# Kernel optimization log

Measured on AMD Instinct MI355X. Metric: run time of the kernel, lower is better.

Reference implementation:

```python
import jax, jax.numpy as jnp
import numpy as np

DIM = 384
HEADS = 12
WH, WW = 8, 10
N = WH * WW  # tokens per window


def _rel_tables():
    # continuous relative coords table, log-spaced (Swin-v2 style, as in source)
    ch = np.arange(-(WH - 1), WH, dtype=np.float32)
    cw = np.arange(-(WW - 1), WW, dtype=np.float32)
    t = np.stack(np.meshgrid(ch, cw, indexing='ij'), axis=-1)  # (2WH-1, 2WW-1, 2)
    t[..., 0] /= (WH - 1)
    t[..., 1] /= (WW - 1)
    t *= 8.0
    t = np.sign(t) * np.log2(np.abs(t) + 1.0) / np.log2(8.0)
    # relative position index (N, N)
    coords = np.stack(np.meshgrid(np.arange(WH), np.arange(WW), indexing='ij'))
    flat = coords.reshape(2, -1)
    rel = (flat[:, :, None] - flat[:, None, :]).transpose(1, 2, 0)
    rel[..., 0] += WH - 1
    rel[..., 1] += WW - 1
    rel[..., 0] *= 2 * WW - 1
    idx = rel.sum(-1)
    return jnp.asarray(t.reshape(-1, 2)), jnp.asarray(idx.reshape(-1))


def _layernorm(x, g, b):
    m = x.mean(-1, keepdims=True)
    v = ((x - m) ** 2).mean(-1, keepdims=True)
    return (x - m) * jax.lax.rsqrt(v + 1e-5) * g + b


def setup_inputs() -> dict:
    key = jax.random.key(0)
    ks = jax.random.split(key, 8)
    s = 0.02
    return {
        'x': jax.random.normal(ks[0], (16, 96, 120, DIM), jnp.float32),
        'norm1_g': jnp.ones((DIM,), jnp.float32),
        'norm1_b': jnp.zeros((DIM,), jnp.float32),
        'qkv_w': jax.random.normal(ks[1], (3 * DIM, DIM), jnp.float32) * s,
        'q_bias': jnp.zeros((DIM,), jnp.float32),
        'v_bias': jnp.zeros((DIM,), jnp.float32),
        'cpb_w1': jax.random.normal(ks[2], (512, 2), jnp.float32) * s,
        'cpb_b1': jnp.zeros((512,), jnp.float32),
        'cpb_w2': jax.random.normal(ks[3], (HEADS, 512), jnp.float32) * s,
        'proj_w': jax.random.normal(ks[4], (DIM, DIM), jnp.float32) * s,
        'proj_b': jnp.zeros((DIM,), jnp.float32),
        'ls1_g': jnp.full((DIM,), 1e-5, jnp.float32),
        'norm2_g': jnp.ones((DIM,), jnp.float32),
        'norm2_b': jnp.zeros((DIM,), jnp.float32),
        'glu_w': jax.random.normal(ks[5], (2048, DIM), jnp.float32) * s,
        'glu_b': jnp.zeros((2048,), jnp.float32),
        'out_w': jax.random.normal(ks[6], (DIM, 1024), jnp.float32) * s,
        'out_b': jnp.zeros((DIM,), jnp.float32),
        'ls2_g': jnp.full((DIM,), 1e-5, jnp.float32),
    }


def reference(x, norm1_g, norm1_b, qkv_w, q_bias, v_bias, cpb_w1, cpb_b1, cpb_w2,
              proj_w, proj_b, ls1_g, norm2_g, norm2_b, glu_w, glu_b, out_w, out_b, ls2_g):
    B, H, W, C = x.shape
    table, idx = _rel_tables()
    # ---- attention branch: norm -> window partition -> MHSA w/ cpb -> reverse ----
    y = _layernorm(x, norm1_g, norm1_b)
    win = y.reshape(B, H // WH, WH, W // WW, WW, C).transpose(0, 1, 3, 2, 4, 5).reshape(-1, N, C)
    qkv_b = jnp.concatenate([q_bias, jnp.zeros_like(v_bias), v_bias])
    qkv = win @ qkv_w.T + qkv_b                                  # (B_, N, 3C)
    qkv = qkv.reshape(-1, N, 3, HEADS, C // HEADS).transpose(2, 0, 3, 1, 4)
    q, k, v = qkv[0], qkv[1], qkv[2]                             # (B_, h, N, d)
    q = q.astype(jnp.float32)
    k = k.astype(jnp.float32)
    q = q / (jnp.linalg.norm(q, axis=-1, keepdims=True) + 5e-5)  # custom_normalize eps
    k = k / (jnp.linalg.norm(k, axis=-1, keepdims=True) + 5e-5)
    attn = jnp.einsum('bhnd,bhmd->bhnm', q, k)
    # continuous relative-position bias: 2-layer MLP over coords table, then gather
    bias_tab = jax.nn.relu(table @ cpb_w1.T + cpb_b1) @ cpb_w2.T     # (T, heads)
    bias = bias_tab[idx].reshape(N, N, HEADS).transpose(2, 0, 1)     # (heads, N, N)
    attn = jax.nn.softmax(attn + 16.0 * jax.nn.sigmoid(bias)[None], axis=-1).astype(x.dtype)
    o = jnp.einsum('bhnm,bhmd->bhnd', attn, v).transpose(0, 2, 1, 3).reshape(-1, N, C)
    o = o @ proj_w.T + proj_b
    o = o.reshape(B, H // WH, W // WW, WH, WW, C).transpose(0, 1, 3, 2, 4, 5).reshape(B, H, W, C)
    x = x + ls1_g * o
    # ---- gated MLP branch ----
    y = _layernorm(x, norm2_g, norm2_b)
    p = y @ glu_w.T + glu_b
    a, gate = jnp.split(p, 2, axis=-1)
    h = a * jax.nn.gelu(gate, approximate=False)
    x = x + ls2_g * (h @ out_w.T + out_b)
    return x
```

## Files before the change

kernel.cpp:

```cpp
#include <hip/hip_runtime.h>
#include <hip/hip_bf16.h>
#include <stdint.h>
#include <math.h>

using bf16 = __hip_bfloat16;
typedef __attribute__((ext_vector_type(8))) short short8;
typedef __attribute__((ext_vector_type(4))) short short4b;
typedef __attribute__((ext_vector_type(4))) float f32x4;

#define TOK    184320
#define CDIM   384
#define NWIN   2304
#define NTOK   80
#define HEADS  12
#define BK     64

constexpr size_t R0_SZ    = (size_t)TOK * CDIM * 2;
constexpr size_t R0_OFF   = 0;
constexpr size_t Q_OFF    = R0_SZ;
constexpr size_t K_OFF    = Q_OFF + R0_SZ;
constexpr size_t V_OFF    = K_OFF + R0_SZ;
constexpr size_t BIAS_OFF = V_OFF + R0_SZ;
constexpr size_t WQKV_OFF = BIAS_OFF + (size_t)HEADS * 6400 * 4;
constexpr size_t WPROJ_OFF= WQKV_OFF + (size_t)1152 * 384 * 2;
constexpr size_t WGLU_OFF = WPROJ_OFF + (size_t)384 * 384 * 2;
constexpr size_t WOUT_OFF = WGLU_OFF + (size_t)2048 * 384 * 2;

__device__ __forceinline__ float b2f(unsigned short u) {
  return __uint_as_float(((unsigned)u) << 16);
}
__device__ __forceinline__ short f2bs(float x) {
  return (short)__bfloat16_as_ushort(__float2bfloat16(x));
}

__device__ __forceinline__ void gload_lds16(const void* g, void* l) {
  typedef __attribute__((address_space(1))) char gchar;
  typedef __attribute__((address_space(3))) char lchar;
  __builtin_amdgcn_global_load_lds((gchar*)(uintptr_t)g, (lchar*)(uintptr_t)l, 16, 0, 0);
}

__device__ __forceinline__ int xcd_swz(int orig, int nwg) {
  int q = nwg >> 3, r = nwg & 7;
  int xcd = orig & 7, loc = orig >> 3;
  return (xcd < r ? xcd * (q + 1) : r * (q + 1) + (xcd - r) * q) + loc;
}

__device__ __forceinline__ int token_to_winrow(int t) {
  int b  = t / (96 * 120);
  int r  = t - b * (96 * 120);
  int hh = r / 120, ww = r - (r / 120) * 120;
  int win = b * 144 + (hh >> 3) * 12 + (ww / 10);
  int n   = (hh & 7) * 10 + (ww % 10);
  return win * NTOK + n;
}

__device__ __forceinline__ int winrow_to_token(int row) {
  int win = row / NTOK, n = row - win * NTOK;
  int b = win / 144, rem = win - b * 144;
  int hh = (rem / 12) * 8 + n / 10;
  int ww = (rem % 12) * 10 + n % 10;
  return (b * 96 + hh) * 120 + ww;
}

__global__ void cvt_f32_bf16(const float* __restrict__ in, bf16* __restrict__ out, int n) {
  int i = blockIdx.x * 256 + threadIdx.x;
  if (i < n) out[i] = __float2bfloat16(in[i]);
}

__global__ void cpb_bias_kernel(const float* __restrict__ w1, const float* __restrict__ b1,
                                const float* __restrict__ w2, float* __restrict__ biasT) {
  __shared__ float tab[285][12];
  for (int r = threadIdx.x; r < 285; r += blockDim.x) {
    int i = r / 19, j = r - (r / 19) * 19;
    float c0 = 8.0f * (float)(i - 7) / 7.0f;
    float c1 = 8.0f * (float)(j - 9) / 9.0f;
    const float inv3 = 1.0f / 3.0f;
    float t0 = (c0 >= 0.f ? 1.f : -1.f) * log2f(fabsf(c0) + 1.f) * inv3;
    float t1 = (c1 >= 0.f ? 1.f : -1.f) * log2f(fabsf(c1) + 1.f) * inv3;
    float acc[12];
    #pragma unroll
    for (int h = 0; h < 12; h++) acc[h] = 0.f;
    for (int k = 0; k < 512; k++) {
      float hk = fmaxf(w1[2 * k] * t0 + w1[2 * k + 1] * t1 + b1[k], 0.f);
      #pragma unroll
      for (int h = 0; h < 12; h++) acc[h] += hk * w2[h * 512 + k];
    }
    #pragma unroll
    for (int h = 0; h < 12; h++) tab[r][h] = acc[h];
  }
  __syncthreads();
  for (int e = threadIdx.x; e < 6400; e += blockDim.x) {
    int n = e / 80, m = e - (e / 80) * 80;
    int id = (n / 10 - m / 10 + 7) * 19 + (n % 10 - m % 10 + 9);
    #pragma unroll
    for (int h = 0; h < 12; h++) {
      float t = tab[id][h];
      biasT[h * 6400 + m * 80 + n] = 16.0f / (1.0f + __expf(-t));
    }
  }
}

__global__ __launch_bounds__(256)
void ln_kernel(const float* __restrict__ x, const float* __restrict__ g,
               const float* __restrict__ b, bf16* __restrict__ out, int windowed) {
  const int wv = threadIdx.x >> 6, lane = threadIdx.x & 63;
  const int token = blockIdx.x * 4 + wv;
  const float* px = x + (size_t)token * CDIM;
  float v[6];
  float s = 0.f;
  #pragma unroll
  for (int j = 0; j < 6; j++) { v[j] = px[lane + 64 * j]; s += v[j]; }
  #pragma unroll
  for (int off = 32; off; off >>= 1) s += __shfl_xor(s, off);
  const float mean = s * (1.0f / 384.0f);
  float sq = 0.f;
  #pragma unroll
  for (int j = 0; j < 6; j++) { float d = v[j] - mean; sq += d * d; }
  #pragma unroll
  for (int off = 32; off; off >>= 1) sq += __shfl_xor(sq, off);
  const float rs = rsqrtf(sq * (1.0f / 384.0f) + 1e-5f);
  const int rowb = windowed ? token_to_winrow(token) : token;
  bf16* po = out + (size_t)rowb * CDIM;
  #pragma unroll
  for (int j = 0; j < 6; j++) {
    int c = lane + 64 * j;
    po[c] = __float2bfloat16((v[j] - mean) * rs * g[c] + b[c]);
  }
}

__global__ __launch_bounds__(64)
void vtrans_kernel(const bf16* __restrict__ v, bf16* __restrict__ vT) {
  __shared__ unsigned short vt[32][82];
  const int wh = blockIdx.x, t = threadIdx.x;
  const unsigned short* vg = (const unsigned short*)v + (size_t)wh * 2560;
  #pragma unroll
  for (int j = 0; j < 5; j++) {
    int c = (t + 64 * j) * 8;
    short8 u = *(const short8*)(vg + c);
    int n = c >> 5, d = c & 31;
    #pragma unroll
    for (int e = 0; e < 8; e++) vt[d + e][n] = (unsigned short)u[e];
  }
  __syncthreads();
  unsigned int* og = (unsigned int*)((unsigned short*)vT + (size_t)wh * 2560);
  #pragma unroll
  for (int j = 0; j < 20; j++) {
    int p = t + 64 * j;
    int e = p * 2;
    int d = e / 80, kcol = e - (e / 80) * 80;
    og[p] = (unsigned int)vt[d][kcol] | ((unsigned int)vt[d][kcol + 1] << 16);
  }
}

#define STAGE_A(buf, kt)                                                          \
  _Pragma("unroll")                                                               \
  for (int j_ = 0; j_ < 4; j_++) {                                                \
    const int ch_ = j_ * 8 + w;                                                   \
    const int el_ = ch_ * 512 + lane * 8;                                         \
    gload_lds16(Ab + (size_t)(el_ >> 6) * LDA + (kt) + (el_ & 63),                \
                As[buf] + ch_ * 512);                                             \
  }
#define STAGE_B(Bp, Bls, buf, kt)                                                 \
  _Pragma("unroll")                                                               \
  for (int j_ = 0; j_ < 2; j_++) {                                                \
    const int ch_ = j_ * 8 + w;                                                   \
    const int el_ = ch_ * 512 + lane * 8;                                         \
    gload_lds16(Bp + (size_t)(el_ >> 6) * LDA + (kt) + (el_ & 63),                \
                Bls[buf] + ch_ * 512);                                            \
  }

#define FRAG_IDX(base, m16, kk) ((base) + ((m16) + lr) * 64 + (kk) + kg * 8)

#define GEMM2_BODY(K_, NT_)                                                       \
  const int LDA = K_;                                                             \
  const int w = threadIdx.x >> 6, lane = threadIdx.x & 63;                        \
  const int wr = w >> 1, wc = w & 1, lr = lane & 15, kg = lane >> 4;              \
  f32x4 acc[4][4];                                                                \
  _Pragma("unroll")                                                               \
  for (int m = 0; m < 4; m++)                                                     \
    _Pragma("unroll")                                                             \
    for (int n = 0; n < 4; n++) acc[m][n] = (f32x4){0.f, 0.f, 0.f, 0.f};          \
  STAGE_A(0, 0) STAGE_B(Bb, Bs, 0, 0)                                             \
  __syncthreads();                                                                \
  for (int t = 0; t < NT_; t++) {                                                 \
    const int cur = t & 1;                                                        \
    if (t + 1 < NT_) { STAGE_A(cur ^ 1, (t + 1) * BK) STAGE_B(Bb, Bs, cur ^ 1, (t + 1) * BK) } \
    _Pragma("unroll")                                                             \
    for (int kk = 0; kk < BK; kk += 32) {                                         \
      short8 af[4], bfr[4];                                                       \
      _Pragma("unroll")                                                           \
      for (int m = 0; m < 4; m++)                                                 \
        af[m] = *(const short8*)FRAG_IDX(As[cur], wr * 64 + m * 16, kk);          \
      _Pragma("unroll")                                                           \
      for (int n = 0; n < 4; n++)                                                 \
        bfr[n] = *(const short8*)FRAG_IDX(Bs[cur], wc * 64 + n * 16, kk);         \
      _Pragma("unroll")                                                           \
      for (int m = 0; m < 4; m++)                                                 \
        _Pragma("unroll")                                                         \
        for (int n = 0; n < 4; n++)                                               \
          acc[m][n] = __builtin_amdgcn_mfma_f32_16x16x32_bf16(af[m], bfr[n], acc[m][n], 0, 0, 0); \
    }                                                                             \
    if (t + 1 < NT_) __syncthreads();                                             \
  }

__global__ __launch_bounds__(512, 2)
void gemm_qkv_kernel(const bf16* __restrict__ A, const bf16* __restrict__ W,
                     const float* __restrict__ qb, const float* __restrict__ vb,
                     bf16* __restrict__ qo, bf16* __restrict__ ko, bf16* __restrict__ vo) {
  __shared__ bf16 As[2][256 * 64], Bs[2][128 * 64];
  const int nbx = 9;
  const int swz = xcd_swz(blockIdx.x, gridDim.x);
  const int by = swz / nbx, bx = swz - (swz / nbx) * nbx;
  const bf16* Ab = A + (size_t)by * 256 * 384;
  const bf16* Bb = W + (size_t)bx * 128 * 384;
  GEMM2_BODY(384, 6)
  #pragma unroll
  for (int m = 0; m < 4; m++)
    #pragma unroll
    for (int i = 0; i < 4; i++) {
      const int row = by * 256 + wr * 64 + m * 16 + kg * 4 + i;
      const int win = row / NTOK, n = row - win * NTOK;
      #pragma unroll
      for (int nn = 0; nn < 4; nn++) {
        const int col = bx * 128 + wc * 64 + nn * 16 + lr;
        const int which = col / 384;
        const int c = col - which * 384;
        const int head = c >> 5, d = c & 31;
        const size_t idx = (((size_t)win * HEADS + head) * NTOK + n) * 32 + d;
        float val = acc[m][nn][i];
        if (which == 0)      qo[idx] = __float2bfloat16(val + qb[c]);
        else if (which == 2) vo[idx] = __float2bfloat16(val + vb[c]);
        else                 ko[idx] = __float2bfloat16(val);
      }
    }
}

__global__ __launch_bounds__(512, 2)
void gemm_proj_kernel(const bf16* __restrict__ A, const bf16* __restrict__ W,
                      const float* __restrict__ pb, const float* __restrict__ x,
                      const float* __restrict__ ls1, float* __restrict__ out) {
  __shared__ bf16 As[2][256 * 64], Bs[2][128 * 64];
  const int nbx = 3;
  const int swz = xcd_swz(blockIdx.x, gridDim.x);
  const int by = swz / nbx, bx = swz - (swz / nbx) * nbx;
  const bf16* Ab = A + (size_t)by * 256 * 384;
  const bf16* Bb = W + (size_t)bx * 128 * 384;
  GEMM2_BODY(384, 6)
  #pragma unroll
  for (int m = 0; m < 4; m++)
    #pragma unroll
    for (int i = 0; i < 4; i++) {
      const int row = by * 256 + wr * 64 + m * 16 + kg * 4 + i;
      const int t = winrow_to_token(row);
      #pragma unroll
      for (int nn = 0; nn < 4; nn++) {
        const int col = bx * 128 + wc * 64 + nn * 16 + lr;
        const size_t gi = (size_t)t * CDIM + col;
        out[gi] = x[gi] + ls1[col] * (acc[m][nn][i] + pb[col]);
      }
    }
}

__global__ __launch_bounds__(512, 2)
void gemm_out_kernel(const bf16* __restrict__ A, const bf16* __restrict__ W,
                     const float* __restrict__ ob, const float* __restrict__ ls2,
                     float* __restrict__ out) {
  __shared__ bf16 As[2][256 * 64], Bs[2][128 * 64];
  const int nbx = 3;
  const int swz = xcd_swz(blockIdx.x, gridDim.x);
  const int by = swz / nbx, bx = swz - (swz / nbx) * nbx;
  const bf16* Ab = A + (size_t)by * 256 * 1024;
  const bf16* Bb = W + (size_t)bx * 128 * 1024;
  GEMM2_BODY(1024, 16)
  #pragma unroll
  for (int m = 0; m < 4; m++)
    #pragma unroll
    for (int i = 0; i < 4; i++) {
      const int row = by * 256 + wr * 64 + m * 16 + kg * 4 + i;
      #pragma unroll
      for (int nn = 0; nn < 4; nn++) {
        const int col = bx * 128 + wc * 64 + nn * 16 + lr;
        const size_t gi = (size_t)row * CDIM + col;
        out[gi] += ls2[col] * (acc[m][nn][i] + ob[col]);
      }
    }
}

__global__ __launch_bounds__(512, 2)
void gemm_glu_kernel(const bf16* __restrict__ A, const bf16* __restrict__ W,
                     const float* __restrict__ gb, bf16* __restrict__ h) {
  __shared__ bf16 As[2][256 * 64], Ba[2][128 * 64], Bg[2][128 * 64];
  const int nbx = 8;
  const int swz = xcd_swz(blockIdx.x, gridDim.x);
  const int by = swz / nbx, bx = swz - (swz / nbx) * nbx;
  const bf16* Ab = A + (size_t)by * 256 * 384;
  const bf16* Wa = W + (size_t)(bx * 128) * 384;
  const bf16* Wg = W + (size_t)(1024 + bx * 128) * 384;
  const int LDA = 384;
  const int w = threadIdx.x >> 6, lane = threadIdx.x & 63;
  const int wr = w >> 1, wc = w & 1, lr = lane & 15, kg = lane >> 4;
  f32x4 aA[4][4], aG[4][4];
  #pragma unroll
  for (int m = 0; m < 4; m++)
    #pragma unroll
    for (int n = 0; n < 4; n++) {
      aA[m][n] = (f32x4){0.f, 0.f, 0.f, 0.f};
      aG[m][n] = (f32x4){0.f, 0.f, 0.f, 0.f};
    }
  STAGE_A(0, 0) STAGE_B(Wa, Ba, 0, 0) STAGE_B(Wg, Bg, 0, 0)
  __syncthreads();
  for (int t = 0; t < 6; t++) {
    const int cur = t & 1;
    if (t + 1 < 6) {
      STAGE_A(cur ^ 1, (t + 1) * BK)
      STAGE_B(Wa, Ba, cur ^ 1, (t + 1) * BK)
      STAGE_B(Wg, Bg, cur ^ 1, (t + 1) * BK)
    }
    #pragma unroll
    for (int kk = 0; kk < BK; kk += 32) {
      short8 af[4], ba[4], bg2[4];
      #pragma unroll
      for (int m = 0; m < 4; m++)
        af[m] = *(const short8*)FRAG_IDX(As[cur], wr * 64 + m * 16, kk);
      #pragma unroll
      for (int n = 0; n < 4; n++) {
        ba[n]  = *(const short8*)FRAG_IDX(Ba[cur], wc * 64 + n * 16, kk);
        bg2[n] = *(const short8*)FRAG_IDX(Bg[cur], wc * 64 + n * 16, kk);
      }
      #pragma unroll
      for (int m = 0; m < 4; m++)
        #pragma unroll
        for (int n = 0; n < 4; n++) {
          aA[m][n] = __builtin_amdgcn_mfma_f32_16x16x32_bf16(af[m], ba[n],  aA[m][n], 0, 0, 0);
          aG[m][n] = __builtin_amdgcn_mfma_f32_16x16x32_bf16(af[m], bg2[n], aG[m][n], 0, 0, 0);
        }
    }
    if (t + 1 < 6) __syncthreads();
  }
  #pragma unroll
  for (int m = 0; m < 4; m++)
    #pragma unroll
    for (int i = 0; i < 4; i++) {
      const int row = by * 256 + wr * 64 + m * 16 + kg * 4 + i;
      #pragma unroll
      for (int nn = 0; nn < 4; nn++) {
        const int col = bx * 128 + wc * 64 + nn * 16 + lr;
        float a = aA[m][nn][i] + gb[col];
        float g = aG[m][nn][i] + gb[1024 + col];
        float gelu = 0.5f * g * (1.0f + erff(g * 0.70710678118654752f));
        h[(size_t)row * 1024 + col] = __float2bfloat16(a * gelu);
      }
    }
}

__global__ __launch_bounds__(256, 2)
void attn_kernel(const bf16* __restrict__ q, const bf16* __restrict__ k,
                 const bf16* __restrict__ vT, const float* __restrict__ biasT,
                 bf16* __restrict__ o) {
  __shared__ short P_all[4][80 * 104];
  const int wv = threadIdx.x >> 6, lane = threadIdx.x & 63;
  const int lr = lane & 15, kg = lane >> 4;
  const int win = blockIdx.x;
  short* P = &P_all[wv][0];
  #pragma unroll
  for (int j = 0; j < 10; j++) {
    int idx = lane + 64 * j;
    int r = idx >> 3, c = idx & 7;
    *(int*)(P + r * 104 + 80 + c * 2) = 0;
  }
  for (int hh = 0; hh < 3; hh++) {
    const int head = wv * 3 + hh;
    const size_t hb = ((size_t)win * HEADS + head) * 2560;
    short8 qf[5], kf[5];
    #pragma unroll
    for (int t5 = 0; t5 < 5; t5++) {
      const int roff = (t5 * 16 + lr) * 32 + kg * 8;
      {
        short8 u = *(const short8*)((const unsigned short*)q + hb + roff);
        float f[8]; float s = 0.f;
        #pragma unroll
        for (int j2 = 0; j2 < 8; j2++) { float x = b2f((unsigned short)u[j2]); f[j2] = x; s += x * x; }
        s += __shfl_xor(s, 16); s += __shfl_xor(s, 32);
        float sc = 1.0f / (sqrtf(s) + 5e-5f);
        short8 r8;
        #pragma unroll
        for (int j2 = 0; j2 < 8; j2++) r8[j2] = f2bs(f[j2] * sc);
        qf[t5] = r8;
      }
      {
        short8 u = *(const short8*)((const unsigned short*)k + hb + roff);
        float f[8]; float s = 0.f;
        #pragma unroll
        for (int j2 = 0; j2 < 8; j2++) { float x = b2f((unsigned short)u[j2]); f[j2] = x; s += x * x; }
        s += __shfl_xor(s, 16); s += __shfl_xor(s, 32);
        float sc = 1.0f / (sqrtf(s) + 5e-5f);
        short8 r8;
        #pragma unroll
        for (int j2 = 0; j2 < 8; j2++) r8[j2] = f2bs(f[j2] * sc);
        kf[t5] = r8;
      }
    }
    f32x4 st[5][5];
    #pragma unroll
    for (int a = 0; a < 5; a++)
      #pragma unroll
      for (int b = 0; b < 5; b++) st[a][b] = (f32x4){0.f, 0.f, 0.f, 0.f};
    #pragma unroll
    for (int a = 0; a < 5; a++)
      #pragma unroll
      for (int b = 0; b < 5; b++)
        st[a][b] = __builtin_amdgcn_mfma_f32_16x16x32_bf16(kf[a], qf[b], st[a][b], 0, 0, 0);
    const float* bh = biasT + head * 6400;
    #pragma unroll
    for (int a = 0; a < 5; a++)
      #pragma unroll
      for (int b = 0; b < 5; b++)
        #pragma unroll
        for (int i = 0; i < 4; i++)
          st[a][b][i] += bh[(a * 16 + kg * 4 + i) * 80 + b * 16 + lr];
    float inv[5];
    #pragma unroll
    for (int b = 0; b < 5; b++) {
      float mx = -1e30f;
      #pragma unroll
      for (int a = 0; a < 5; a++)
        #pragma unroll
        for (int i = 0; i < 4; i++) mx = fmaxf(mx, st[a][b][i]);
      mx = fmaxf(mx, __shfl_xor(mx, 16));
      mx = fmaxf(mx, __shfl_xor(mx, 32));
      float sm = 0.f;
      #pragma unroll
      for (int a = 0; a < 5; a++)
        #pragma unroll
        for (int i = 0; i < 4; i++) { float e = __expf(st[a][b][i] - mx); st[a][b][i] = e; sm += e; }
      sm += __shfl_xor(sm, 16); sm += __shfl_xor(sm, 32);
      inv[b] = 1.0f / sm;
    }
    #pragma unroll
    for (int a = 0; a < 5; a++)
      #pragma unroll
      for (int b = 0; b < 5; b++) {
        short4b pk;
        #pragma unroll
        for (int i = 0; i < 4; i++) pk[i] = f2bs(st[a][b][i] * inv[b]);
        *(short4b*)(P + (b * 16 + lr) * 104 + a * 16 + kg * 4) = pk;
      }
    const unsigned short* vh = (const unsigned short*)vT + hb;
    short8 vf[2][3];
    #pragma unroll
    for (int dt = 0; dt < 2; dt++)
      #pragma unroll
      for (int ks = 0; ks < 3; ks++) {
        const int kb = ks * 32 + ((ks == 2 && kg >= 2) ? 0 : kg * 8);
        vf[dt][ks] = *(const short8*)(vh + (dt * 16 + lr) * 80 + kb);
      }
    f32x4 oc[5][2];
    #pragma unroll
    for (int b = 0; b < 5; b++)
      #pragma unroll
      for (int dt = 0; dt < 2; dt++) oc[b][dt] = (f32x4){0.f, 0.f, 0.f, 0.f};
    #pragma unroll
    for (int b = 0; b < 5; b++) {
      short8 pa[3];
      #pragma unroll
      for (int ks = 0; ks < 3; ks++)
        pa[ks] = *(const short8*)(P + (b * 16 + lr) * 104 + ks * 32 + kg * 8);
      #pragma unroll
      for (int dt = 0; dt < 2; dt++)
        #pragma unroll
        for (int ks = 0; ks < 3; ks++)
          oc[b][dt] = __builtin_amdgcn_mfma_f32_16x16x32_bf16(pa[ks], vf[dt][ks], oc[b][dt], 0, 0, 0);
    }
    unsigned short* ob = (unsigned short*)o + (size_t)win * NTOK * CDIM + head * 32;
    #pragma unroll
    for (int b = 0; b < 5; b++)
      #pragma unroll
      for (int i = 0; i < 4; i++) {
        const int row = b * 16 + kg * 4 + i;
        #pragma unroll
        for (int dt = 0; dt < 2; dt++)
          ob[(size_t)row * CDIM + dt * 16 + lr] = (unsigned short)f2bs(oc[b][dt][i]);
      }
  }
}

extern "C" void kernel_launch(void* const* d_in, const int* in_sizes, int n_in,
                              void* d_out, int out_size, void* d_ws, size_t ws_size,
                              hipStream_t stream) {
  const float* x       = (const float*)d_in[0];
  const float* n1g     = (const float*)d_in[1];
  const float* n1b     = (const float*)d_in[2];
  const float* qkv_w   = (const float*)d_in[3];
  const float* q_bias  = (const float*)d_in[4];
  const float* v_bias  = (const float*)d_in[5];
  const float* cpb_w1  = (const float*)d_in[6];
  const float* cpb_b1  = (const float*)d_in[7];
  const float* cpb_w2  = (const float*)d_in[8];
  const float* proj_w  = (const float*)d_in[9];
  const float* proj_b  = (const float*)d_in[10];
  const float* ls1     = (const float*)d_in[11];
  const float* n2g     = (const float*)d_in[12];
  const float* n2b     = (const float*)d_in[13];
  const float* glu_w   = (const float*)d_in[14];
  const float* glu_b   = (const float*)d_in[15];
  const float* out_w   = (const float*)d_in[16];
  const float* out_b   = (const float*)d_in[17];
  const float* ls2     = (const float*)d_in[18];
  float* out = (float*)d_out;

  char* ws = (char*)d_ws;
  bf16* r0     = (bf16*)(ws + R0_OFF);
  bf16* q_buf  = (bf16*)(ws + Q_OFF);
  bf16* k_buf  = (bf16*)(ws + K_OFF);
  bf16* v_buf  = (bf16*)(ws + V_OFF);
  bf16* h_buf  = (bf16*)(ws + Q_OFF);
  float* biasT = (float*)(ws + BIAS_OFF);
  bf16* wqkv   = (bf16*)(ws + WQKV_OFF);
  bf16* wproj  = (bf16*)(ws + WPROJ_OFF);
  bf16* wglu   = (bf16*)(ws + WGLU_OFF);
  bf16* wout   = (bf16*)(ws + WOUT_OFF);

  cvt_f32_bf16<<<dim3((1152 * 384 + 255) / 256), 256, 0, stream>>>(qkv_w, wqkv, 1152 * 384);
  cvt_f32_bf16<<<dim3((384 * 384 + 255) / 256), 256, 0, stream>>>(proj_w, wproj, 384 * 384);
  cvt_f32_bf16<<<dim3((2048 * 384 + 255) / 256), 256, 0, stream>>>(glu_w, wglu, 2048 * 384);
  cvt_f32_bf16<<<dim3((384 * 1024 + 255) / 256), 256, 0, stream>>>(out_w, wout, 384 * 1024);

  cpb_bias_kernel<<<1, 256, 0, stream>>>(cpb_w1, cpb_b1, cpb_w2, biasT);

  ln_kernel<<<TOK / 4, 256, 0, stream>>>(x, n1g, n1b, r0, 1);

  gemm_qkv_kernel<<<720 * 9, 512, 0, stream>>>(r0, wqkv, q_bias, v_bias, q_buf, k_buf, v_buf);

  vtrans_kernel<<<NWIN * HEADS, 64, 0, stream>>>(v_buf, r0);

  attn_kernel<<<NWIN, 256, 0, stream>>>(q_buf, k_buf, r0, biasT, v_buf);

  gemm_proj_kernel<<<720 * 3, 512, 0, stream>>>(v_buf, wproj, proj_b, x, ls1, out);

  ln_kernel<<<TOK / 4, 256, 0, stream>>>(out, n2g, n2b, r0, 0);

  gemm_glu_kernel<<<720 * 8, 512, 0, stream>>>(r0, wglu, glu_b, h_buf);

  gemm_out_kernel<<<720 * 3, 512, 0, stream>>>(h_buf, wout, out_b, ls2, out);

  (void)in_sizes; (void)n_in; (void)out_size; (void)ws_size;
}
```

Before: 2.620 ms.

## Triple-buffer GEMM LDS pipeline with XOR swizzle and halve GLU row tile

Replaces double-buffered LDS staging in the four GEMM kernels with a three-stage ring. It waits with explicit vmcnt waits and s_barrier instead of __syncthreads each step, so global loads for tile t+2 overlap compute on tile t. Source columns are XOR-swizzled by row, which is meant to cut LDS bank conflicts on fragment reads. MFMA blocks are wrapped in s_setprio to favour the math waves. The GLU kernel moves to 128-row tiles and a doubled grid to keep triple-buffer LDS usage at two blocks per CU, which costs more reloads of the weight tiles.

```diff
diff --git a/kernel.cpp b/kernel.cpp
--- a/kernel.cpp
+++ b/kernel.cpp
@@ -61,6 +61,8 @@
   int ww = (rem % 12) * 10 + n % 10;
   return (b * 96 + hh) * 120 + ww;
 }
+
+#define SWZ_COL(c_, r_) ((c_) ^ (((r_) & 7) << 3))
 
 __global__ void cvt_f32_bf16(const float* __restrict__ in, bf16* __restrict__ out, int n) {
   int i = blockIdx.x * 256 + threadIdx.x;
@@ -152,26 +154,50 @@
   }
 }
 
-#define STAGE_A(buf, kt)                                                          \
+#define STAGE3_A(buf, kt)                                                         \
   _Pragma("unroll")                                                               \
   for (int j_ = 0; j_ < 4; j_++) {                                                \
     const int ch_ = j_ * 8 + w;                                                   \
     const int el_ = ch_ * 512 + lane * 8;                                         \
-    gload_lds16(Ab + (size_t)(el_ >> 6) * LDA + (kt) + (el_ & 63),                \
-                As[buf] + ch_ * 512);                                             \
-  }
-#define STAGE_B(Bp, Bls, buf, kt)                                                 \
+    const int r_ = el_ >> 6, c_ = el_ & 63;                                       \
+    gload_lds16(Ab + (size_t)r_ * LDA + (kt) + SWZ_COL(c_, r_),                   \
+                As3 + (buf) * (256 * 64) + ch_ * 512);                            \
+  }
+#define STAGE3_B(Bp, Bls, nb_, buf, kt)                                           \
   _Pragma("unroll")                                                               \
-  for (int j_ = 0; j_ < 2; j_++) {                                                \
+  for (int j_ = 0; j_ < (nb_); j_++) {                                            \
     const int ch_ = j_ * 8 + w;                                                   \
     const int el_ = ch_ * 512 + lane * 8;                                         \
-    gload_lds16(Bp + (size_t)(el_ >> 6) * LDA + (kt) + (el_ & 63),                \
-                Bls[buf] + ch_ * 512);                                            \
-  }
-
-#define FRAG_IDX(base, m16, kk) ((base) + ((m16) + lr) * 64 + (kk) + kg * 8)
-
-#define GEMM2_BODY(K_, NT_)                                                       \
+    const int r_ = el_ >> 6, c_ = el_ & 63;                                       \
+    gload_lds16(Bp + (size_t)r_ * LDA + (kt) + SWZ_COL(c_, r_),                   \
+                Bls + (buf) * (128 * 64) + ch_ * 512);                            \
+  }
+
+#define COMPUTE3(buf)                                                             \
+  {                                                                               \
+    const bf16* A_ = As3 + (buf) * (256 * 64);                                    \
+    const bf16* B_ = Bs3 + (buf) * (128 * 64);                                    \
+    _Pragma("unroll")                                                             \
+    for (int kk = 0; kk < BK; kk += 32) {                                         \
+      const int cs_ = SWZ_COL(kk + kg * 8, lr);                                   \
+      short8 af[4], bfr[4];                                                       \
+      _Pragma("unroll")                                                           \
+      for (int m = 0; m < 4; m++)                                                 \
+        af[m] = *(const short8*)(A_ + (wr * 64 + m * 16 + lr) * 64 + cs_);        \
+      _Pragma("unroll")                                                           \
+      for (int n = 0; n < 4; n++)                                                 \
+        bfr[n] = *(const short8*)(B_ + (wc * 64 + n * 16 + lr) * 64 + cs_);       \
+      __builtin_amdgcn_s_setprio(1);                                              \
+      _Pragma("unroll")                                                           \
+      for (int m = 0; m < 4; m++)                                                 \
+        _Pragma("unroll")                                                         \
+        for (int n = 0; n < 4; n++)                                               \
+          acc[m][n] = __builtin_amdgcn_mfma_f32_16x16x32_bf16(af[m], bfr[n], acc[m][n], 0, 0, 0); \
+      __builtin_amdgcn_s_setprio(0);                                              \
+    }                                                                             \
+  }
+
+#define GEMM3_BODY(K_, NT_)                                                       \
   const int LDA = K_;                                                             \
   const int w = threadIdx.x >> 6, lane = threadIdx.x & 63;                        \
   const int wr = w >> 1, wc = w & 1, lr = lane & 15, kg = lane >> 4;              \
@@ -180,40 +206,34 @@
   for (int m = 0; m < 4; m++)                                                     \
     _Pragma("unroll")                                                             \
     for (int n = 0; n < 4; n++) acc[m][n] = (f32x4){0.f, 0.f, 0.f, 0.f};          \
-  STAGE_A(0, 0) STAGE_B(Bb, Bs, 0, 0)                                             \
-  __syncthreads();                                                                \
-  for (int t = 0; t < NT_; t++) {                                                 \
-    const int cur = t & 1;                                                        \
-    if (t + 1 < NT_) { STAGE_A(cur ^ 1, (t + 1) * BK) STAGE_B(Bb, Bs, cur ^ 1, (t + 1) * BK) } \
-    _Pragma("unroll")                                                             \
-    for (int kk = 0; kk < BK; kk += 32) {                                         \
-      short8 af[4], bfr[4];                                                       \
-      _Pragma("unroll")                                                           \
-      for (int m = 0; m < 4; m++)                                                 \
-        af[m] = *(const short8*)FRAG_IDX(As[cur], wr * 64 + m * 16, kk);          \
-      _Pragma("unroll")                                                           \
-      for (int n = 0; n < 4; n++)                                                 \
-        bfr[n] = *(const short8*)FRAG_IDX(Bs[cur], wc * 64 + n * 16, kk);         \
-      _Pragma("unroll")                                                           \
-      for (int m = 0; m < 4; m++)                                                 \
-        _Pragma("unroll")                                                         \
-        for (int n = 0; n < 4; n++)                                               \
-          acc[m][n] = __builtin_amdgcn_mfma_f32_16x16x32_bf16(af[m], bfr[n], acc[m][n], 0, 0, 0); \
+  STAGE3_A(0, 0) STAGE3_B(Bb, Bs3, 2, 0, 0)                                       \
+  STAGE3_A(1, BK) STAGE3_B(Bb, Bs3, 2, 1, BK)                                     \
+  _Pragma("unroll")                                                               \
+  for (int t = 0; t < NT_ - 1; t++) {                                             \
+    asm volatile("s_waitcnt vmcnt(6)" ::: "memory");                              \
+    __builtin_amdgcn_s_barrier();                                                 \
+    if (t + 2 < NT_) {                                                            \
+      STAGE3_A((t + 2) % 3, (t + 2) * BK)                                         \
+      STAGE3_B(Bb, Bs3, 2, (t + 2) % 3, (t + 2) * BK)                             \
     }                                                                             \
-    if (t + 1 < NT_) __syncthreads();                                             \
-  }
+    COMPUTE3(t % 3)                                                               \
+  }                                                                               \
+  asm volatile("s_waitcnt vmcnt(0)" ::: "memory");                                \
+  __builtin_amdgcn_s_barrier();                                                   \
+  COMPUTE3((NT_ - 1) % 3)
 
 __global__ __launch_bounds__(512, 2)
 void gemm_qkv_kernel(const bf16* __restrict__ A, const bf16* __restrict__ W,
                      const float* __restrict__ qb, const float* __restrict__ vb,
                      bf16* __restrict__ qo, bf16* __restrict__ ko, bf16* __restrict__ vo) {
-  __shared__ bf16 As[2][256 * 64], Bs[2][128 * 64];
+  __shared__ __align__(16) bf16 As3[3 * 256 * 64];
+  __shared__ __align__(16) bf16 Bs3[3 * 128 * 64];
   const int nbx = 9;
   const int swz = xcd_swz(blockIdx.x, gridDim.x);
   const int by = swz / nbx, bx = swz - (swz / nbx) * nbx;
   const bf16* Ab = A + (size_t)by * 256 * 384;
   const bf16* Bb = W + (size_t)bx * 128 * 384;
-  GEMM2_BODY(384, 6)
+  GEMM3_BODY(384, 6)
   #pragma unroll
   for (int m = 0; m < 4; m++)
     #pragma unroll
@@ -239,13 +259,14 @@
 void gemm_proj_kernel(const bf16* __restrict__ A, const bf16* __restrict__ W,
                       const float* __restrict__ pb, const float* __restrict__ x,
                       const float* __restrict__ ls1, float* __restrict__ out) {
-  __shared__ bf16 As[2][256 * 64], Bs[2][128 * 64];
+  __shared__ __align__(16) bf16 As3[3 * 256 * 64];
+  __shared__ __align__(16) bf16 Bs3[3 * 128 * 64];
   const int nbx = 3;
   const int swz = xcd_swz(blockIdx.x, gridDim.x);
   const int by = swz / nbx, bx = swz - (swz / nbx) * nbx;
   const bf16* Ab = A + (size_t)by * 256 * 384;
   const bf16* Bb = W + (size_t)bx * 128 * 384;
-  GEMM2_BODY(384, 6)
+  GEMM3_BODY(384, 6)
   #pragma unroll
   for (int m = 0; m < 4; m++)
     #pragma unroll
@@ -265,13 +286,14 @@
 void gemm_out_kernel(const bf16* __restrict__ A, const bf16* __restrict__ W,
                      const float* __restrict__ ob, const float* __restrict__ ls2,
                      float* __restrict__ out) {
-  __shared__ bf16 As[2][256 * 64], Bs[2][128 * 64];
+  __shared__ __align__(16) bf16 As3[3 * 256 * 64];
+  __shared__ __align__(16) bf16 Bs3[3 * 128 * 64];
   const int nbx = 3;
   const int swz = xcd_swz(blockIdx.x, gridDim.x);
   const int by = swz / nbx, bx = swz - (swz / nbx) * nbx;
   const bf16* Ab = A + (size_t)by * 256 * 1024;
   const bf16* Bb = W + (size_t)bx * 128 * 1024;
-  GEMM2_BODY(1024, 16)
+  GEMM3_BODY(1024, 16)
   #pragma unroll
   for (int m = 0; m < 4; m++)
     #pragma unroll
@@ -289,59 +311,99 @@
 __global__ __launch_bounds__(512, 2)
 void gemm_glu_kernel(const bf16* __restrict__ A, const bf16* __restrict__ W,
                      const float* __restrict__ gb, bf16* __restrict__ h) {
-  __shared__ bf16 As[2][256 * 64], Ba[2][128 * 64], Bg[2][128 * 64];
+  __shared__ __align__(16) bf16 Asl[3 * 128 * 64];
+  __shared__ __align__(16) bf16 Bal[3 * 128 * 64];
+  __shared__ __align__(16) bf16 Bgl[3 * 128 * 64];
   const int nbx = 8;
   const int swz = xcd_swz(blockIdx.x, gridDim.x);
   const int by = swz / nbx, bx = swz - (swz / nbx) * nbx;
-  const bf16* Ab = A + (size_t)by * 256 * 384;
+  const bf16* Ab = A + (size_t)by * 128 * 384;
   const bf16* Wa = W + (size_t)(bx * 128) * 384;
   const bf16* Wg = W + (size_t)(1024 + bx * 128) * 384;
   const int LDA = 384;
   const int w = threadIdx.x >> 6, lane = threadIdx.x & 63;
   const int wr = w >> 1, wc = w & 1, lr = lane & 15, kg = lane >> 4;
-  f32x4 aA[4][4], aG[4][4];
-  #pragma unroll
-  for (int m = 0; m < 4; m++)
+  f32x4 aA[2][4], aG[2][4];
+  #pragma unroll
+  for (int m = 0; m < 2; m++)
     #pragma unroll
     for (int n = 0; n < 4; n++) {
       aA[m][n] = (f32x4){0.f, 0.f, 0.f, 0.f};
       aG[m][n] = (f32x4){0.f, 0.f, 0.f, 0.f};
     }
-  STAGE_A(0, 0) STAGE_B(Wa, Ba, 0, 0) STAGE_B(Wg, Bg, 0, 0)
-  __syncthreads();
-  for (int t = 0; t < 6; t++) {
-    const int cur = t & 1;
-    if (t + 1 < 6) {
-      STAGE_A(cur ^ 1, (t + 1) * BK)
-      STAGE_B(Wa, Ba, cur ^ 1, (t + 1) * BK)
-      STAGE_B(Wg, Bg, cur ^ 1, (t + 1) * BK)
-    }
+  STAGE3_B(Ab, Asl, 2, 0, 0) STAGE3_B(Wa, Bal, 2, 0, 0) STAGE3_B(Wg, Bgl, 2, 0, 0)
+  STAGE3_B(Ab, Asl, 2, 1, BK) STAGE3_B(Wa, Bal, 2, 1, BK) STAGE3_B(Wg, Bgl, 2, 1, BK)
+  #pragma unroll
+  for (int t = 0; t < 5; t++) {
+    asm volatile("s_waitcnt vmcnt(6)" ::: "memory");
+    __builtin_amdgcn_s_barrier();
+    if (t + 2 < 6) {
+      STAGE3_B(Ab, Asl, 2, (t + 2) % 3, (t + 2) * BK)
+      STAGE3_B(Wa, Bal, 2, (t + 2) % 3, (t + 2) * BK)
+      STAGE3_B(Wg, Bgl, 2, (t + 2) % 3, (t + 2) * BK)
+    }
+    {
+      const bf16* A_ = Asl + (t % 3) * (128 * 64);
+      const bf16* Ba_ = Bal + (t % 3) * (128 * 64);
+      const bf16* Bg_ = Bgl + (t % 3) * (128 * 64);
+      #pragma unroll
+      for (int kk = 0; kk < BK; kk += 32) {
+        const int cs_ = SWZ_COL(kk + kg * 8, lr);
+        short8 af[2], ba[4], bg2[4];
+        #pragma unroll
+        for (int m = 0; m < 2; m++)
+          af[m] = *(const short8*)(A_ + (wr * 32 + m * 16 + lr) * 64 + cs_);
+        #pragma unroll
+        for (int n = 0; n < 4; n++) {
+          ba[n]  = *(const short8*)(Ba_ + (wc * 64 + n * 16 + lr) * 64 + cs_);
+          bg2[n] = *(const short8*)(Bg_ + (wc * 64 + n * 16 + lr) * 64 + cs_);
+        }
+        __builtin_amdgcn_s_setprio(1);
+        #pragma unroll
+        for (int m = 0; m < 2; m++)
+          #pragma unroll
+          for (int n = 0; n < 4; n++) {
+            aA[m][n] = __builtin_amdgcn_mfma_f32_16x16x32_bf16(af[m], ba[n],  aA[m][n], 0, 0, 0);
+            aG[m][n] = __builtin_amdgcn_mfma_f32_16x16x32_bf16(af[m], bg2[n], aG[m][n], 0, 0, 0);
+          }
+        __builtin_amdgcn_s_setprio(0);
+      }
+    }
+  }
+  asm volatile("s_waitcnt vmcnt(0)" ::: "memory");
+  __builtin_amdgcn_s_barrier();
+  {
+    const bf16* A_ = Asl + (5 % 3) * (128 * 64);
+    const bf16* Ba_ = Bal + (5 % 3) * (128 * 64);
+    const bf16* Bg_ = Bgl + (5 % 3) * (128 * 64);
     #pragma unroll
     for (int kk = 0; kk < BK; kk += 32) {
-      short8 af[4], ba[4], bg2[4];
-      #pragma unroll
-      for (int m = 0; m < 4; m++)
-        af[m] = *(const short8*)FRAG_IDX(As[cur], wr * 64 + m * 16, kk);
+      const int cs_ = SWZ_COL(kk + kg * 8, lr);
+      short8 af[2], ba[4], bg2[4];
+      #pragma unroll
+      for (int m = 0; m < 2; m++)
+        af[m] = *(const short8*)(A_ + (wr * 32 + m * 16 + lr) * 64 + cs_);
       #pragma unroll
       for (int n = 0; n < 4; n++) {
-        ba[n]  = *(const short8*)FRAG_IDX(Ba[cur], wc * 64 + n * 16, kk);
-        bg2[n] = *(const short8*)FRAG_IDX(Bg[cur], wc * 64 + n * 16, kk);
-      }
-      #pragma unroll
-      for (int m = 0; m < 4; m++)
+        ba[n]  = *(const short8*)(Ba_ + (wc * 64 + n * 16 + lr) * 64 + cs_);
+        bg2[n] = *(const short8*)(Bg_ + (wc * 64 + n * 16 + lr) * 64 + cs_);
+      }
+      __builtin_amdgcn_s_setprio(1);
+      #pragma unroll
+      for (int m = 0; m < 2; m++)
         #pragma unroll
         for (int n = 0; n < 4; n++) {
           aA[m][n] = __builtin_amdgcn_mfma_f32_16x16x32_bf16(af[m], ba[n],  aA[m][n], 0, 0, 0);
           aG[m][n] = __builtin_amdgcn_mfma_f32_16x16x32_bf16(af[m], bg2[n], aG[m][n], 0, 0, 0);
         }
-    }
-    if (t + 1 < 6) __syncthreads();
-  }
-  #pragma unroll
-  for (int m = 0; m < 4; m++)
+      __builtin_amdgcn_s_setprio(0);
+    }
+  }
+  #pragma unroll
+  for (int m = 0; m < 2; m++)
     #pragma unroll
     for (int i = 0; i < 4; i++) {
-      const int row = by * 256 + wr * 64 + m * 16 + kg * 4 + i;
+      const int row = by * 128 + wr * 32 + m * 16 + kg * 4 + i;
       #pragma unroll
       for (int nn = 0; nn < 4; nn++) {
         const int col = bx * 128 + wc * 64 + nn * 16 + lr;
@@ -539,7 +601,7 @@
 
   ln_kernel<<<TOK / 4, 256, 0, stream>>>(out, n2g, n2b, r0, 0);
 
-  gemm_glu_kernel<<<720 * 8, 512, 0, stream>>>(r0, wglu, glu_b, h_buf);
+  gemm_glu_kernel<<<1440 * 8, 512, 0, stream>>>(r0, wglu, glu_b, h_buf);
 
   gemm_out_kernel<<<720 * 3, 512, 0, stream>>>(h_buf, wout, out_b, ls2, out);
 
```

Result: faster. 2.515 ms (-4.0%).
